# Optimization experiments

Hardware: AMD Instinct MI355X
Metric: run time of the kernel (lower is better)

## Reference

```python
import jax, jax.numpy as jnp
import numpy as np

VAR0, VAR1 = 0.1, 0.2       # variances used by encode()
THRESH = 0.35               # overlap_thresh
NEGPOS = 7                  # negpos_ratio


def point_form(p):
    # (cx,cy,w,h) -> (xmin,ymin,xmax,ymax)
    return jnp.concatenate([p[:, :2] - p[:, 2:] / 2, p[:, :2] + p[:, 2:] / 2], axis=1)


def jaccard(a, b):
    # a:[G,4], b:[P,4] corner form -> IoU [G,P]
    lt = jnp.maximum(a[:, None, :2], b[None, :, :2])
    rb = jnp.minimum(a[:, None, 2:], b[None, :, 2:])
    wh = jnp.clip(rb - lt, 0.0, None)
    inter = wh[..., 0] * wh[..., 1]
    area_a = (a[:, 2] - a[:, 0]) * (a[:, 3] - a[:, 1])
    area_b = (b[:, 2] - b[:, 0]) * (b[:, 3] - b[:, 1])
    return inter / (area_a[:, None] + area_b[None, :] - inter)


def encode(matched, priors):
    g_cxcy = ((matched[:, :2] + matched[:, 2:]) / 2 - priors[:, :2]) / (VAR0 * priors[:, 2:])
    g_wh = jnp.log((matched[:, 2:] - matched[:, :2]) / priors[:, 2:]) / VAR1
    return jnp.concatenate([g_cxcy, g_wh], axis=1)


def encode_landm(matched, priors):
    m = matched.reshape(-1, 5, 2)                                  # [P,5,2]
    g = (m - priors[:, None, :2]) / (VAR0 * priors[:, None, 2:])
    return g.reshape(-1, 10)


def match_one(truths, labels, landms, priors, priors_pf):
    # truths:[G,4] labels:[G] landms:[G,10] priors:[P,4](cxcywh) priors_pf:[P,4](corner)
    G = truths.shape[0]
    P = priors.shape[0]
    ov = jaccard(truths, priors_pf)                                # [G,P]
    best_prior_ov = ov.max(axis=1)                                 # [G]
    best_prior_idx = ov.argmax(axis=1)                             # [G]
    valid_gt = best_prior_ov >= 0.2
    best_truth_ov = ov.max(axis=0)                                 # [P]
    best_truth_idx = ov.argmax(axis=0)                             # [P]
    # index_fill_(0, best_prior_idx[valid_gt], 2): 2 > any IoU, so max is equivalent
    forced_ov = jnp.zeros((P,), ov.dtype).at[best_prior_idx].max(jnp.where(valid_gt, 2.0, 0.0))
    best_truth_ov = jnp.maximum(best_truth_ov, forced_ov)
    forced_idx = jnp.full((P,), -1, jnp.int32).at[best_prior_idx].max(jnp.arange(G, dtype=jnp.int32))
    best_truth_idx = jnp.where(forced_idx >= 0, forced_idx, best_truth_idx.astype(jnp.int32))
    conf = labels[best_truth_idx].astype(jnp.int32)
    conf = jnp.where(best_truth_ov < THRESH, 0, conf)
    loc = encode(truths[best_truth_idx], priors)                   # [P,4]
    landm = encode_landm(landms[best_truth_idx], priors)           # [P,10]
    # if no valid gt, torch zeroes the targets for this sample
    any_valid = valid_gt.any()
    loc = jnp.where(any_valid, loc, 0.0)
    landm = jnp.where(any_valid, landm, 0.0)
    conf = jnp.where(any_valid, conf, 0)
    return loc, conf, landm


def smooth_l1(x):
    ax = jnp.abs(x)
    return jnp.where(ax < 1.0, 0.5 * ax * ax, ax - 0.5)


def setup_inputs() -> dict:
    key = jax.random.key(0)
    k1, k2, k3, k4, k5, k6, k7, k8, k9 = jax.random.split(key, 9)
    B, P, G, C = 64, 16800, 32, 2
    cls_data = jax.random.normal(k1, (B, P, C), jnp.float32)
    loc_data = jax.random.normal(k2, (B, P, 4), jnp.float32)
    landm_data = jax.random.normal(k3, (B, P, 10), jnp.float32)
    # priors in (cx,cy,w,h), w,h in [0.02,0.3]
    pc = jax.random.uniform(k4, (P, 2), jnp.float32)
    pwh = jax.random.uniform(k5, (P, 2), jnp.float32, 0.02, 0.3)
    priors = jnp.concatenate([pc, pwh], axis=1)
    # targets: [B,G,15] = 4 box (corner form, valid) + 10 landmarks + 1 label
    c = jax.random.uniform(k6, (B, G, 2), jnp.float32, 0.15, 0.85)
    s = jax.random.uniform(k7, (B, G, 2), jnp.float32, 0.02, 0.3)
    boxes = jnp.concatenate([c - s / 2, c + s / 2], axis=-1)
    lms = jax.random.uniform(k8, (B, G, 10), jnp.float32)
    labels = jnp.where(jax.random.uniform(k9, (B, G, 1)) < 0.3, -1.0, 1.0)
    targets = jnp.concatenate([boxes, lms, labels], axis=-1)
    return {"cls_data": cls_data, "loc_data": loc_data, "landm_data": landm_data,
            "priors": priors, "targets": targets}


def reference(cls_data, loc_data, landm_data, priors, targets):
    truths = targets[:, :, :4]
    landms = targets[:, :, 4:14]
    labels = targets[:, :, 14]
    priors_pf = point_form(priors)
    loc_t, conf_t, landm_t = jax.vmap(
        lambda t, l, lm: match_one(t, l, lm, priors, priors_pf))(truths, labels, landms)
    num, P = conf_t.shape

    # landmark loss (smooth L1 over conf_t > 0)
    pos1 = conf_t > 0
    N1 = jnp.maximum(pos1.sum().astype(jnp.float32), 1.0)
    loss_landm = jnp.sum(smooth_l1(landm_data - landm_t) * pos1[..., None].astype(landm_data.dtype))

    # localization loss (smooth L1 over conf_t != 0)
    pos = conf_t != 0
    conf_t = jnp.where(pos, 1, conf_t)                              # conf_t[pos] = 1
    loss_l = jnp.sum(smooth_l1(loc_data - loc_t) * pos[..., None].astype(loc_data.dtype))

    # hard negative mining on per-prior CE loss
    logz = jax.nn.logsumexp(cls_data, axis=-1)                      # [B,P]
    gold = jnp.take_along_axis(cls_data, conf_t[..., None], axis=-1)[..., 0]
    loss_c = jnp.where(pos, 0.0, logz - gold)
    loss_idx = jnp.argsort(-loss_c, axis=1)
    idx_rank = jnp.argsort(loss_idx, axis=1)
    num_pos = pos.sum(axis=1, keepdims=True)
    num_neg = jnp.clip(NEGPOS * num_pos, None, P - 1)
    neg = idx_rank < num_neg

    sel = (pos | neg).astype(cls_data.dtype)
    loss_conf = jnp.sum((logz - gold) * sel)

    N = jnp.maximum(num_pos.sum().astype(jnp.float32), 1.0)
    return loss_l / N, loss_conf / N, loss_landm / N1
```

## Files before the change

### kernel.cpp

```cpp
#include <hip/hip_runtime.h>
#include <hip/hip_bf16.h>
#include <math.h>


#define RCP(x) __builtin_amdgcn_rcpf(x)

constexpr int GN = 32;

__device__ __forceinline__ float sl1(float x) {
    float a = fabsf(x);
    return a < 1.f ? 0.5f * a * a : a - 0.5f;
}

constexpr int GPB = 4;
constexpr int GNT = 512;
__global__ __launch_bounds__(GNT)
void k_gt(const float4* __restrict__ priors, const float* __restrict__ targets,
          unsigned long long* __restrict__ keys, int P, int G) {
    const int b = blockIdx.y, g0 = blockIdx.x * GPB, tid = threadIdx.x;
    const int lane = tid & 63, w = tid >> 6;
    __shared__ float4 s_box[GPB];
    __shared__ float  s_at[GPB];
    __shared__ unsigned long long s_wk[GNT / 64][GPB];
    if (tid < GPB) {
        const float* t = targets + ((size_t)b * G + g0 + tid) * 15;
        float4 v = make_float4(t[0], t[1], t[2], t[3]);
        s_box[tid] = v;
        s_at[tid] = (v.z - v.x) * (v.w - v.y);
    }
    __syncthreads();
    float4 tb0 = s_box[0], tb1 = s_box[1], tb2 = s_box[2], tb3 = s_box[3];
    float at0 = s_at[0], at1 = s_at[1], at2 = s_at[2], at3 = s_at[3];

    float bv[GPB]; int bp[GPB];
    #pragma unroll
    for (int j = 0; j < GPB; ++j) { bv[j] = -1.f; bp[j] = 0; }

    for (int p = tid; p < P; p += GNT) {
        float4 pr = priors[p];
        float hx = pr.z * 0.5f, hy = pr.w * 0.5f;
        float px0 = pr.x - hx, py0 = pr.y - hy;
        float px1 = pr.x + hx, py1 = pr.y + hy;
        float ap = (px1 - px0) * (py1 - py0);
        #pragma unroll
        for (int j = 0; j < GPB; ++j) {
            float4 tb = j == 0 ? tb0 : (j == 1 ? tb1 : (j == 2 ? tb2 : tb3));
            float at = j == 0 ? at0 : (j == 1 ? at1 : (j == 2 ? at2 : at3));
            float lx = fmaxf(tb.x, px0), ly = fmaxf(tb.y, py0);
            float rx = fminf(tb.z, px1), ry = fminf(tb.w, py1);
            float iw = fmaxf(rx - lx, 0.f), ih = fmaxf(ry - ly, 0.f);
            float inter = iw * ih;
            float iou = inter * RCP(at + ap - inter);
            if (iou > bv[j]) { bv[j] = iou; bp[j] = p; }
        }
    }
    #pragma unroll
    for (int j = 0; j < GPB; ++j) {
        unsigned long long key =
            ((unsigned long long)__float_as_uint(bv[j]) << 32) | ~(unsigned)bp[j];
        #pragma unroll
        for (int o = 32; o > 0; o >>= 1) {
            unsigned long long t = __shfl_down(key, o, 64);
            if (t > key) key = t;
        }
        if (lane == 0) s_wk[w][j] = key;
    }
    __syncthreads();
    if (tid < GPB) {
        unsigned long long m = 0ull;
        #pragma unroll
        for (int q = 0; q < GNT / 64; ++q) { unsigned long long t = s_wk[q][tid]; if (t > m) m = t; }
        keys[b * G + g0 + tid] = m;
    }
}

__global__ __launch_bounds__(256)
void k_match(const float2* __restrict__ cls, const float4* __restrict__ loc,
             const float* __restrict__ lmd, const float4* __restrict__ priors,
             const float* __restrict__ targets,
             const unsigned long long* __restrict__ keys,
             float* __restrict__ bc, float* __restrict__ part, int P, int NB) {
    const int b = blockIdx.y, bx = blockIdx.x, tid = threadIdx.x;
    const int lane = tid & 63, w = tid >> 6;
    __shared__ float s_t[GN * 4];
    __shared__ float s_at[GN];
    __shared__ float s_lm[GN * 10];
    __shared__ float s_lab[GN];
    __shared__ unsigned s_kl[GN];
    __shared__ unsigned s_vm;
    __shared__ float s_red[4][8];
    for (int i = tid; i < GN * 15; i += 256) {
        int g = i / 15, j = i - g * 15;
        float v = targets[((size_t)b * GN + g) * 15 + j];
        if (j < 4) s_t[g * 4 + j] = v;
        else if (j < 14) s_lm[g * 10 + (j - 4)] = v;
        else s_lab[g] = v;
    }
    bool gvalid = false;
    if (tid < GN) {
        unsigned long long key = keys[b * GN + tid];
        s_kl[tid] = (unsigned)key;
        gvalid = __uint_as_float((unsigned)(key >> 32)) >= 0.2f;
    }
    if (w == 0) {
        unsigned long long bal = __ballot(gvalid);
        if (tid == 0) s_vm = (unsigned)bal;
    }
    __syncthreads();
    if (tid < GN)
        s_at[tid] = (s_t[tid * 4 + 2] - s_t[tid * 4]) * (s_t[tid * 4 + 3] - s_t[tid * 4 + 1]);
    __syncthreads();
    const unsigned vm = s_vm;
    const bool av = vm != 0;

    int p = bx * 256 + tid;
    float a_ll = 0.f, a_lm = 0.f, a_lcp = 0.f, a_np = 0.f, a_np1 = 0.f;
    if (p < P) {
        float4 pr = priors[p];
        float hx = pr.z * 0.5f, hy = pr.w * 0.5f;
        float px0 = pr.x - hx, py0 = pr.y - hy;
        float px1 = pr.x + hx, py1 = pr.y + hy;
        float ap = (px1 - px0) * (py1 - py0);
        float btv = -1.f; int bti_ = 0;
        #pragma unroll
        for (int g = 0; g < GN; ++g) {
            float lx = fmaxf(s_t[g * 4], px0), ly = fmaxf(s_t[g * 4 + 1], py0);
            float rx = fminf(s_t[g * 4 + 2], px1), ry = fminf(s_t[g * 4 + 3], py1);
            float iw = fmaxf(rx - lx, 0.f), ih = fmaxf(ry - ly, 0.f);
            float inter = iw * ih;
            float iou = inter * RCP(s_at[g] + ap - inter);
            if (iou > btv) { btv = iou; bti_ = g; }
        }
        unsigned npk = ~(unsigned)p;
        int fidx = -1; bool fv = false;
        #pragma unroll
        for (int g = 0; g < GN; ++g)
            if (s_kl[g] == npk) { fidx = g; fv = fv || ((vm >> g) & 1u); }
        int bti2 = fidx >= 0 ? fidx : bti_;
        bool pos = av && (fv || btv >= 0.35f);
        float lab = s_lab[bti2];

        float2 c = cls[(size_t)b * P + p];
        float d = c.y - c.x, m0 = fmaxf(d, 0.f);
        float lse = m0 + __logf(__expf(-m0) + __expf(d - m0));
        bc[(size_t)b * P + p] = pos ? 0.f : lse;

        if (pos) {
            a_np = 1.f;
            a_lcp = lse - d;
            float tx0 = s_t[bti2 * 4], ty0 = s_t[bti2 * 4 + 1];
            float tx1 = s_t[bti2 * 4 + 2], ty1 = s_t[bti2 * 4 + 3];
            float rw = RCP(pr.z), rh = RCP(pr.w);
            float e0 = ((tx0 + tx1) * 0.5f - pr.x) * rw * 10.f;
            float e1 = ((ty0 + ty1) * 0.5f - pr.y) * rh * 10.f;
            float e2 = __logf((tx1 - tx0) * rw) * 5.f;
            float e3 = __logf((ty1 - ty0) * rh) * 5.f;
            float4 ld = loc[(size_t)b * P + p];
            a_ll = sl1(ld.x - e0) + sl1(ld.y - e1) + sl1(ld.z - e2) + sl1(ld.w - e3);
            if (lab > 0.f) {
                a_np1 = 1.f;
                const float* lp = lmd + ((size_t)b * P + p) * 10;
                #pragma unroll
                for (int q = 0; q < 5; ++q) {
                    float gx = (s_lm[bti2 * 10 + 2 * q]     - pr.x) * rw * 10.f;
                    float gy = (s_lm[bti2 * 10 + 2 * q + 1] - pr.y) * rh * 10.f;
                    a_lm += sl1(lp[2 * q] - gx) + sl1(lp[2 * q + 1] - gy);
                }
            }
        }
    }
    #pragma unroll
    for (int o = 32; o > 0; o >>= 1) {
        a_ll  += __shfl_down(a_ll,  o, 64);
        a_lm  += __shfl_down(a_lm,  o, 64);
        a_lcp += __shfl_down(a_lcp, o, 64);
        a_np  += __shfl_down(a_np,  o, 64);
        a_np1 += __shfl_down(a_np1, o, 64);
    }
    if (lane == 0) {
        s_red[w][0] = a_ll; s_red[w][1] = a_lm; s_red[w][2] = a_lcp;
        s_red[w][3] = a_np; s_red[w][4] = a_np1;
    }
    __syncthreads();
    if (tid == 0) {
        float* pp = part + ((size_t)b * NB + bx) * 8;
        #pragma unroll
        for (int j = 0; j < 5; ++j)
            pp[j] = s_red[0][j] + s_red[1][j] + s_red[2][j] + s_red[3][j];
    }
}

constexpr int SNT = 1024;
constexpr int SNI = 17;
__global__ __launch_bounds__(SNT)
void k_select(const float* __restrict__ bc, const float* __restrict__ part,
              float* __restrict__ part2, int P, int NB) {
    const int b = blockIdx.x, tid = threadIdx.x;
    const int lane = tid & 63, w = tid >> 6;
    unsigned ul[SNI];
    #pragma unroll
    for (int i = 0; i < SNI; ++i) {
        int idx = i * SNT + tid;
        ul[i] = idx < P ? __float_as_uint(bc[(size_t)b * P + idx]) : 0u;
    }
    __shared__ float s_r[5];
    if (w < 5) {
        float s = 0.f;
        for (int bx = lane; bx < NB; bx += 64) s += part[((size_t)b * NB + bx) * 8 + w];
        #pragma unroll
        for (int o = 32; o > 0; o >>= 1) s += __shfl_down(s, o, 64);
        if (lane == 0) s_r[w] = s;
    }
    __syncthreads();
    float t_ll = s_r[0], t_lm = s_r[1], t_lcp = s_r[2], t_np = s_r[3], t_np1 = s_r[4];
    int np = (int)(t_np + 0.5f);
    int k = np * 7;
    if (k > P - 1) k = P - 1;

    __shared__ int s_ri[16];
    __shared__ int s_i0;
    __shared__ float s_rf[16];
    float topk = 0.f;
    if (k > 0) {
        unsigned lo = 0u, hi = 0x7f800000u;
        while (lo < hi) {
            unsigned mid = lo + ((hi - lo + 1) >> 1);
            int cnt = 0;
            #pragma unroll
            for (int i = 0; i < SNI; ++i) cnt += (ul[i] >= mid) ? 1 : 0;
            #pragma unroll
            for (int o = 32; o > 0; o >>= 1) cnt += __shfl_down(cnt, o, 64);
            if (lane == 0) s_ri[w] = cnt;
            __syncthreads();
            if (tid == 0) {
                int r = 0;
                #pragma unroll
                for (int q = 0; q < 16; ++q) r += s_ri[q];
                s_i0 = r;
            }
            __syncthreads();
            if (s_i0 >= k) lo = mid; else hi = mid - 1;
        }
        float fT = __uint_as_float(lo);
        float s = 0.f; int c = 0;
        #pragma unroll
        for (int i = 0; i < SNI; ++i)
            if (ul[i] > lo) { s += __uint_as_float(ul[i]); c++; }
        #pragma unroll
        for (int o = 32; o > 0; o >>= 1) {
            s += __shfl_down(s, o, 64);
            c += __shfl_down(c, o, 64);
        }
        if (lane == 0) { s_rf[w] = s; s_ri[w] = c; }
        __syncthreads();
        if (tid == 0) {
            float ts = 0.f; int tc = 0;
            #pragma unroll
            for (int q = 0; q < 16; ++q) { ts += s_rf[q]; tc += s_ri[q]; }
            topk = ts + (float)(k - tc) * fT;
        }
    }
    if (tid == 0) {
        float* pp = part2 + b * 8;
        pp[0] = t_ll; pp[1] = t_lm; pp[2] = t_lcp;
        pp[3] = topk; pp[4] = t_np; pp[5] = t_np1;
    }
}

__global__ void k_final(const float* __restrict__ part2, float* __restrict__ out, int B) {
    int lane = threadIdx.x;
    float ll = 0, lm = 0, lcp = 0, tk = 0, np = 0, np1 = 0;
    for (int b = lane; b < B; b += 64) {
        const float* pp = part2 + b * 8;
        ll += pp[0]; lm += pp[1]; lcp += pp[2];
        tk += pp[3]; np += pp[4]; np1 += pp[5];
    }
    #pragma unroll
    for (int o = 32; o > 0; o >>= 1) {
        ll  += __shfl_down(ll, o, 64);
        lm  += __shfl_down(lm, o, 64);
        lcp += __shfl_down(lcp, o, 64);
        tk  += __shfl_down(tk, o, 64);
        np  += __shfl_down(np, o, 64);
        np1 += __shfl_down(np1, o, 64);
    }
    if (lane == 0) {
        float N = fmaxf(np, 1.f), N1 = fmaxf(np1, 1.f);
        out[0] = ll / N;
        out[1] = (lcp + tk) / N;
        out[2] = lm / N1;
    }
}

extern "C" void kernel_launch(void* const* d_in, const int* in_sizes, int n_in,
                              void* d_out, int out_size, void* d_ws, size_t ws_size,
                              hipStream_t stream) {
    const float2* cls    = (const float2*)d_in[0];
    const float4* loc    = (const float4*)d_in[1];
    const float* lmd     = (const float*)d_in[2];
    const float4* priors = (const float4*)d_in[3];
    const float* targets = (const float*)d_in[4];
    int P = in_sizes[3] / 4;
    int B = (in_sizes[1] / 4) / P;
    int NB = (P + 255) / 256;
    int G = in_sizes[4] / (15 * B);

    size_t off = 0;
    unsigned long long* keys = (unsigned long long*)d_ws; off += (size_t)B * G * 8;
    float* part  = (float*)((char*)d_ws + off); off += (size_t)B * NB * 8 * 4;
    float* part2 = (float*)((char*)d_ws + off); off += (size_t)B * 8 * 4;
    off = (off + 255) & ~(size_t)255;
    float* bc = (float*)((char*)d_ws + off);

    dim3 ggt((G + GPB - 1) / GPB, B);
    k_gt<<<ggt, GNT, 0, stream>>>(priors, targets, keys, P, G);
    dim3 gm(NB, B);
    k_match<<<gm, 256, 0, stream>>>(cls, loc, lmd, priors, targets, keys, bc, part, P, NB);
    k_select<<<B, SNT, 0, stream>>>(bc, part, part2, P, NB);
    k_final<<<1, 64, 0, stream>>>(part2, (float*)d_out, B);
}
```

Before: 89.91 us.

## Cull GT boxes per wavefront and defer argmax IoU to positive priors

The matching kernel now computes each wavefront's prior bounding box and ballots which ground-truth boxes overlap it, so the IoU loop only visits those candidates. The positive test is done without division by comparing 1.35*inter - 0.35*area_t against 0.35*area_p. The full argmax IoU is computed only for positive priors that have no forced match. The per-prior scan over the 32 keys is replaced by a shared-memory scatter with atomicMax, and the positive counts come from ballot/popcount. This saves ALU and reciprocal work in the hot loop, at the cost of divergent loops and extra shared memory and syncs.

```diff
diff --git a/kernel.cpp b/kernel.cpp
--- a/kernel.cpp
+++ b/kernel.cpp
@@ -82,104 +82,146 @@
              float* __restrict__ bc, float* __restrict__ part, int P, int NB) {
     const int b = blockIdx.y, bx = blockIdx.x, tid = threadIdx.x;
     const int lane = tid & 63, w = tid >> 6;
-    __shared__ float s_t[GN * 4];
-    __shared__ float s_at[GN];
-    __shared__ float s_lm[GN * 10];
-    __shared__ float s_lab[GN];
-    __shared__ unsigned s_kl[GN];
+    __shared__ float4 s_box[GN];
+    __shared__ float  s_at[GN];
+    __shared__ float  s_c035[GN];
+    __shared__ float  s_lm[GN * 10];
+    __shared__ float  s_lab[GN];
+    __shared__ int    s_fg[256];
+    __shared__ int    s_fv[256];
     __shared__ unsigned s_vm;
-    __shared__ float s_red[4][8];
+    __shared__ float  s_red[4][8];
+
+    s_fg[tid] = -1; s_fv[tid] = 0;
     for (int i = tid; i < GN * 15; i += 256) {
         int g = i / 15, j = i - g * 15;
         float v = targets[((size_t)b * GN + g) * 15 + j];
-        if (j < 4) s_t[g * 4 + j] = v;
+        if (j < 4) ((float*)&s_box[g])[j] = v;
         else if (j < 14) s_lm[g * 10 + (j - 4)] = v;
         else s_lab[g] = v;
     }
-    bool gvalid = false;
+    __syncthreads();
     if (tid < GN) {
+        float4 v = s_box[tid];
+        float at = (v.z - v.x) * (v.w - v.y);
+        s_at[tid] = at;
+        s_c035[tid] = 0.35f * at;
         unsigned long long key = keys[b * GN + tid];
-        s_kl[tid] = (unsigned)key;
-        gvalid = __uint_as_float((unsigned)(key >> 32)) >= 0.2f;
-    }
-    if (w == 0) {
-        unsigned long long bal = __ballot(gvalid);
+        unsigned bp = ~(unsigned)key;
+        bool val = __uint_as_float((unsigned)(key >> 32)) >= 0.2f;
+        unsigned long long bal = __ballot(val);
         if (tid == 0) s_vm = (unsigned)bal;
-    }
-    __syncthreads();
-    if (tid < GN)
-        s_at[tid] = (s_t[tid * 4 + 2] - s_t[tid * 4]) * (s_t[tid * 4 + 3] - s_t[tid * 4 + 1]);
-    __syncthreads();
-    const unsigned vm = s_vm;
-    const bool av = vm != 0;
+        int local = (int)bp - bx * 256;
+        if (local >= 0 && local < 256) {
+            atomicMax(&s_fg[local], tid);
+            if (val) atomicOr(&s_fv[local], 1);
+        }
+    }
+    __syncthreads();
+    const bool av = s_vm != 0u;
+    const int  fidx = s_fg[tid];
+    const bool fv = s_fv[tid] != 0;
 
     int p = bx * 256 + tid;
-    float a_ll = 0.f, a_lm = 0.f, a_lcp = 0.f, a_np = 0.f, a_np1 = 0.f;
-    if (p < P) {
-        float4 pr = priors[p];
-        float hx = pr.z * 0.5f, hy = pr.w * 0.5f;
-        float px0 = pr.x - hx, py0 = pr.y - hy;
-        float px1 = pr.x + hx, py1 = pr.y + hy;
-        float ap = (px1 - px0) * (py1 - py0);
-        float btv = -1.f; int bti_ = 0;
-        #pragma unroll
-        for (int g = 0; g < GN; ++g) {
-            float lx = fmaxf(s_t[g * 4], px0), ly = fmaxf(s_t[g * 4 + 1], py0);
-            float rx = fminf(s_t[g * 4 + 2], px1), ry = fminf(s_t[g * 4 + 3], py1);
-            float iw = fmaxf(rx - lx, 0.f), ih = fmaxf(ry - ly, 0.f);
-            float inter = iw * ih;
-            float iou = inter * RCP(s_at[g] + ap - inter);
-            if (iou > btv) { btv = iou; bti_ = g; }
-        }
-        unsigned npk = ~(unsigned)p;
-        int fidx = -1; bool fv = false;
-        #pragma unroll
-        for (int g = 0; g < GN; ++g)
-            if (s_kl[g] == npk) { fidx = g; fv = fv || ((vm >> g) & 1u); }
-        int bti2 = fidx >= 0 ? fidx : bti_;
-        bool pos = av && (fv || btv >= 0.35f);
-        float lab = s_lab[bti2];
-
+    const bool act = p < P;
+    float4 pr = act ? priors[p] : make_float4(0.f, 0.f, 0.f, 0.f);
+    float hx = pr.z * 0.5f, hy = pr.w * 0.5f;
+    float px0 = pr.x - hx, py0 = pr.y - hy;
+    float px1 = pr.x + hx, py1 = pr.y + hy;
+    float ap = (px1 - px0) * (py1 - py0);
+    if (!act) { px0 = py0 = INFINITY; px1 = py1 = -INFINITY; }
+
+    float wx0 = px0, wy0 = py0, wx1 = px1, wy1 = py1;
+    #pragma unroll
+    for (int o = 32; o > 0; o >>= 1) {
+        wx0 = fminf(wx0, __shfl_xor(wx0, o, 64));
+        wy0 = fminf(wy0, __shfl_xor(wy0, o, 64));
+        wx1 = fmaxf(wx1, __shfl_xor(wx1, o, 64));
+        wy1 = fmaxf(wy1, __shfl_xor(wy1, o, 64));
+    }
+    bool sg = false;
+    if (lane < GN) {
+        float4 tb = s_box[lane];
+        sg = (tb.x < wx1) && (tb.z > wx0) && (tb.y < wy1) && (tb.w > wy0);
+    }
+    unsigned mask = (unsigned)__ballot(sg);
+
+    float qmax = -INFINITY;
+    unsigned m2 = mask;
+    while (m2) {
+        int g = __ffs(m2) - 1; m2 &= m2 - 1;
+        float4 tb = s_box[g];
+        float lx = fmaxf(tb.x, px0), ly = fmaxf(tb.y, py0);
+        float rx = fminf(tb.z, px1), ry = fminf(tb.w, py1);
+        float iw = fmaxf(rx - lx, 0.f), ih = fmaxf(ry - ly, 0.f);
+        float inter = iw * ih;
+        qmax = fmaxf(qmax, fmaf(1.35f, inter, -s_c035[g]));
+    }
+    bool thr = act && (qmax >= 0.35f * ap);
+    bool pos = act && av && (fv || thr);
+
+    float lse = 0.f, d = 0.f;
+    if (act) {
         float2 c = cls[(size_t)b * P + p];
-        float d = c.y - c.x, m0 = fmaxf(d, 0.f);
-        float lse = m0 + __logf(__expf(-m0) + __expf(d - m0));
+        d = c.y - c.x;
+        float m0 = fmaxf(d, 0.f);
+        lse = m0 + __logf(__expf(-m0) + __expf(d - m0));
         bc[(size_t)b * P + p] = pos ? 0.f : lse;
-
-        if (pos) {
-            a_np = 1.f;
-            a_lcp = lse - d;
-            float tx0 = s_t[bti2 * 4], ty0 = s_t[bti2 * 4 + 1];
-            float tx1 = s_t[bti2 * 4 + 2], ty1 = s_t[bti2 * 4 + 3];
-            float rw = RCP(pr.z), rh = RCP(pr.w);
-            float e0 = ((tx0 + tx1) * 0.5f - pr.x) * rw * 10.f;
-            float e1 = ((ty0 + ty1) * 0.5f - pr.y) * rh * 10.f;
-            float e2 = __logf((tx1 - tx0) * rw) * 5.f;
-            float e3 = __logf((ty1 - ty0) * rh) * 5.f;
-            float4 ld = loc[(size_t)b * P + p];
-            a_ll = sl1(ld.x - e0) + sl1(ld.y - e1) + sl1(ld.z - e2) + sl1(ld.w - e3);
-            if (lab > 0.f) {
-                a_np1 = 1.f;
-                const float* lp = lmd + ((size_t)b * P + p) * 10;
-                #pragma unroll
-                for (int q = 0; q < 5; ++q) {
-                    float gx = (s_lm[bti2 * 10 + 2 * q]     - pr.x) * rw * 10.f;
-                    float gy = (s_lm[bti2 * 10 + 2 * q + 1] - pr.y) * rh * 10.f;
-                    a_lm += sl1(lp[2 * q] - gx) + sl1(lp[2 * q + 1] - gy);
-                }
+    }
+
+    float a_ll = 0.f, a_lm = 0.f, a_lcp = 0.f;
+    bool posl = false;
+    if (pos) {
+        a_lcp = lse - d;
+        int bti2 = fidx;
+        if (fidx < 0) {
+            float btv = -1.f;
+            unsigned m3 = mask;
+            while (m3) {
+                int g = __ffs(m3) - 1; m3 &= m3 - 1;
+                float4 tb = s_box[g];
+                float lx = fmaxf(tb.x, px0), ly = fmaxf(tb.y, py0);
+                float rx = fminf(tb.z, px1), ry = fminf(tb.w, py1);
+                float iw = fmaxf(rx - lx, 0.f), ih = fmaxf(ry - ly, 0.f);
+                float inter = iw * ih;
+                float iou = inter * RCP(s_at[g] + ap - inter);
+                if (iou > btv) { btv = iou; bti2 = g; }
             }
         }
-    }
-    #pragma unroll
-    for (int o = 32; o > 0; o >>= 1) {
-        a_ll  += __shfl_down(a_ll,  o, 64);
-        a_lm  += __shfl_down(a_lm,  o, 64);
-        a_lcp += __shfl_down(a_lcp, o, 64);
-        a_np  += __shfl_down(a_np,  o, 64);
-        a_np1 += __shfl_down(a_np1, o, 64);
+        float4 tb = s_box[bti2];
+        float rw = RCP(pr.z), rh = RCP(pr.w);
+        float e0 = ((tb.x + tb.z) * 0.5f - pr.x) * rw * 10.f;
+        float e1 = ((tb.y + tb.w) * 0.5f - pr.y) * rh * 10.f;
+        float e2 = __logf((tb.z - tb.x) * rw) * 5.f;
+        float e3 = __logf((tb.w - tb.y) * rh) * 5.f;
+        float4 ld = loc[(size_t)b * P + p];
+        a_ll = sl1(ld.x - e0) + sl1(ld.y - e1) + sl1(ld.z - e2) + sl1(ld.w - e3);
+        if (s_lab[bti2] > 0.f) {
+            posl = true;
+            const float* lp = lmd + ((size_t)b * P + p) * 10;
+            #pragma unroll
+            for (int q = 0; q < 5; ++q) {
+                float gx = (s_lm[bti2 * 10 + 2 * q]     - pr.x) * rw * 10.f;
+                float gy = (s_lm[bti2 * 10 + 2 * q + 1] - pr.y) * rh * 10.f;
+                a_lm += sl1(lp[2 * q] - gx) + sl1(lp[2 * q + 1] - gy);
+            }
+        }
+    }
+
+    unsigned long long bpos = __ballot(pos);
+    int npw  = __popcll(bpos);
+    int np1w = __popcll(__ballot(posl));
+    if (bpos) {
+        #pragma unroll
+        for (int o = 32; o > 0; o >>= 1) {
+            a_ll  += __shfl_down(a_ll,  o, 64);
+            a_lm  += __shfl_down(a_lm,  o, 64);
+            a_lcp += __shfl_down(a_lcp, o, 64);
+        }
     }
     if (lane == 0) {
         s_red[w][0] = a_ll; s_red[w][1] = a_lm; s_red[w][2] = a_lcp;
-        s_red[w][3] = a_np; s_red[w][4] = a_np1;
+        s_red[w][3] = (float)npw; s_red[w][4] = (float)np1w;
     }
     __syncthreads();
     if (tid == 0) {
```

Result: slower. 96.60 us (+7.4%).
